# Performance work log

Hardware: AMD Instinct MI355X
Metric: run time of the kernel (lower is better)

## Reference

```python
import jax, jax.numpy as jnp
import numpy as np

D_MODEL = 1024
N_HEAD = 16


def setup_inputs() -> dict:
    key = jax.random.key(0)
    ks = jax.random.split(key, 12)
    B, T, D = 2, 2048, D_MODEL
    s = 1.0 / np.sqrt(D)
    return {
        "q": jax.random.normal(ks[0], (B, T, D), jnp.float32),
        "k": jax.random.normal(ks[1], (B, T, D), jnp.float32),
        "v": jax.random.normal(ks[2], (B, T, D), jnp.float32),
        "w_q": jax.random.normal(ks[3], (D, D), jnp.float32) * s,
        "b_q": jnp.zeros((D,), jnp.float32),
        "w_k": jax.random.normal(ks[4], (D, D), jnp.float32) * s,
        "b_k": jnp.zeros((D,), jnp.float32),
        "w_v": jax.random.normal(ks[5], (D, D), jnp.float32) * s,
        "b_v": jnp.zeros((D,), jnp.float32),
        "w_o": jax.random.normal(ks[6], (D, D), jnp.float32) * s,
        "b_o": jnp.zeros((D,), jnp.float32),
    }


def reference(q, k, v, w_q, b_q, w_k, b_k, w_v, b_v, w_o, b_o):
    B, T, D = q.shape
    H = N_HEAD
    nd = D // H  # head dim
    # projections (weights stored as [in, out])
    qh = (q @ w_q + b_q).reshape(B, T, H, nd).transpose(0, 2, 1, 3)  # [b,h,t,nd]
    kh = (k @ w_k + b_k).reshape(B, T, H, nd).transpose(0, 2, 1, 3)
    vh = (v @ w_v + b_v).reshape(B, T, H, nd).transpose(0, 2, 1, 3)
    score = jnp.einsum('bhqd,bhkd->bhqk', qh, kh) / jnp.sqrt(jnp.float32(nd))
    causal = jnp.tril(jnp.ones((T, T), dtype=bool))  # [tq, tk]
    score = jnp.where(causal, score, -jnp.inf)
    # NOTE: original module uses nn.Softmax(dim=-2), i.e. softmax over the
    # QUERY axis. Faithful to the source.
    attn = jax.nn.softmax(score, axis=-2)
    out = jnp.einsum('bhqk,bhkd->bhqd', attn, vh)  # [b,h,t,nd]
    out = out.transpose(0, 2, 1, 3).reshape(B, T, D)
    return out @ w_o + b_o
```

## Files before the change

### kernel.cpp

```cpp
#include <hip/hip_runtime.h>
#include <hip/hip_bf16.h>
#include <cstdint>
#include <cstddef>

#define D_MODEL 1024
#define NHEAD   16
#define HDIM    64
#define BB      2
#define TT      2048
#define MM      (BB*TT)
#define BHN     (BB*NHEAD)

typedef __attribute__((ext_vector_type(8))) __bf16 bf16x8;
typedef __attribute__((ext_vector_type(4))) float  f32x4;
typedef __attribute__((ext_vector_type(8))) unsigned short u16x8;
typedef __attribute__((ext_vector_type(4))) unsigned short u16x4;

__device__ __forceinline__ unsigned short f2b(float f){
  __bf16 b = (__bf16)f;
  return __builtin_bit_cast(unsigned short, b);
}
__device__ __forceinline__ float b2f(unsigned short u){
  unsigned int x = ((unsigned int)u) << 16;
  return __builtin_bit_cast(float, x);
}

__device__ __forceinline__ f32x4 mfma16(bf16x8 a, bf16x8 b, f32x4 c){
  return __builtin_amdgcn_mfma_f32_16x16x32_bf16(a, b, c, 0, 0, 0);
}

__device__ __forceinline__ void gload16(const void* g, void* lds){
  __builtin_amdgcn_global_load_lds((const __attribute__((address_space(1))) void*)g,
                                   (__attribute__((address_space(3))) void*)lds, 16, 0, 0);
}

__global__ void cvt_bf16_kernel(const float* __restrict__ q, const float* __restrict__ k,
                                const float* __restrict__ v,
                                unsigned short* __restrict__ Xq, unsigned short* __restrict__ Xk,
                                unsigned short* __restrict__ Xv){
  const int z = blockIdx.y;
  const float* x = z==0 ? q : z==1 ? k : v;
  unsigned short* y = z==0 ? Xq : z==1 ? Xk : Xv;
  size_t i = (size_t)blockIdx.x*blockDim.x + threadIdx.x;
  const float4* p = (const float4*)(x + i*8);
  float4 a = p[0], b = p[1];
  u16x8 o;
  o[0]=f2b(a.x); o[1]=f2b(a.y); o[2]=f2b(a.z); o[3]=f2b(a.w);
  o[4]=f2b(b.x); o[5]=f2b(b.y); o[6]=f2b(b.z); o[7]=f2b(b.w);
  *(u16x8*)(y + i*8) = o;
}

__global__ void transpose_w_kernel(const float* __restrict__ W0, const float* __restrict__ W1,
                                   const float* __restrict__ W2, const float* __restrict__ W3,
                                   unsigned short* __restrict__ T0, unsigned short* __restrict__ T1,
                                   unsigned short* __restrict__ T2, unsigned short* __restrict__ T3){
  __shared__ float tile[32][33];
  const int z = blockIdx.z;
  const float* W = z==0 ? W0 : z==1 ? W1 : z==2 ? W2 : W3;
  unsigned short* Wt = z==0 ? T0 : z==1 ? T1 : z==2 ? T2 : T3;
  int tx = threadIdx.x, ty = threadIdx.y;
  int x0 = blockIdx.x*32, y0 = blockIdx.y*32;
  #pragma unroll
  for (int i=0;i<4;i++)
    tile[ty + i*8][tx] = W[(size_t)(y0 + ty + i*8)*D_MODEL + x0 + tx];
  __syncthreads();
  #pragma unroll
  for (int i=0;i<4;i++)
    Wt[(size_t)(x0 + ty + i*8)*D_MODEL + y0 + tx] = f2b(tile[tx][ty + i*8]);
}

__device__ __forceinline__ void gemm_body(const unsigned short* __restrict__ A,
                                          const unsigned short* __restrict__ Bt,
                                          const float* __restrict__ bias,
                                          void* __restrict__ Cout, const int mode,
                                          const int m0, const int n0)
{
  constexpr int K = D_MODEL, N = D_MODEL;
  __shared__ unsigned short As[3][128*32];
  __shared__ unsigned short Bs[3][128*32];
  const int t = threadIdx.x, lane = t&63, w = t>>6;
  const int wr = w>>1, wc = w&1, lr = lane&15, lg = lane>>4;
  const int srow = lane>>2;
  const int schunk = (lane&3) ^ ((lane>>3)&3);
  const int crd = lg ^ ((lr>>1)&3);
  f32x4 acc[4][4] = {};

  auto stage = [&](int buf, int ks){
    int k0 = ks*32;
    #pragma unroll
    for (int g=0; g<2; g++){
      int reg = w*2 + g;
      int r = reg*16 + srow;
      gload16(A  + (size_t)(m0+r)*K + k0 + schunk*8, (char*)As[buf] + reg*1024);
      gload16(Bt + (size_t)(n0+r)*K + k0 + schunk*8, (char*)Bs[buf] + reg*1024);
    }
  };

  stage(0, 0);
  stage(1, 1);
  asm volatile("s_waitcnt vmcnt(4)" ::: "memory");
  asm volatile("s_barrier" ::: "memory");

  int bi = 0;
  for (int ks = 0; ks < 32; ++ks){
    if (ks + 2 < 32){
      int nb = bi + 2; if (nb >= 3) nb -= 3;
      stage(nb, ks+2);
    }
    const char* bufA = (const char*)As[bi];
    const char* bufB = (const char*)Bs[bi];
    bf16x8 af[4], bfv[4];
    #pragma unroll
    for (int mi=0;mi<4;mi++){
      int r = wr*64 + mi*16 + lr;
      af[mi] = *(const bf16x8*)(bufA + r*64 + crd*16);
    }
    #pragma unroll
    for (int ni=0;ni<4;ni++){
      int r = wc*64 + ni*16 + lr;
      bfv[ni] = *(const bf16x8*)(bufB + r*64 + crd*16);
    }
    #pragma unroll
    for (int mi=0;mi<4;mi++)
      #pragma unroll
      for (int ni=0;ni<4;ni++)
        acc[mi][ni] = mfma16(af[mi], bfv[ni], acc[mi][ni]);
    if (ks < 30) asm volatile("s_waitcnt vmcnt(4)" ::: "memory");
    else         asm volatile("s_waitcnt vmcnt(0)" ::: "memory");
    asm volatile("s_barrier" ::: "memory");
    bi = (bi == 2) ? 0 : bi + 1;
  }

  #pragma unroll
  for (int mi=0;mi<4;mi++){
    #pragma unroll
    for (int ni=0;ni<4;ni++){
      int n = n0 + wc*64 + ni*16 + lr;
      int mbase = m0 + wr*64 + mi*16 + lg*4;
      float bv = bias[n];
      if (mode == 0){
        unsigned short* Cb = (unsigned short*)Cout;
        #pragma unroll
        for (int r=0;r<4;r++) Cb[(size_t)(mbase+r)*N + n] = f2b(acc[mi][ni][r] + bv);
      } else {
        unsigned short* Vt = (unsigned short*)Cout;
        int h = n >> 6, d = n & 63;
        int b = mbase >> 11;
        int tq = mbase & (TT-1);
        u16x4 vv;
        #pragma unroll
        for (int r=0;r<4;r++) vv[r] = f2b(acc[mi][ni][r] + bv);
        *(u16x4*)(Vt + ((size_t)((b*NHEAD + h)*HDIM + d))*TT + tq) = vv;
      }
    }
  }
}

__launch_bounds__(256)
__global__ void proj_gemm_kernel(const unsigned short* __restrict__ Xq,
                                 const unsigned short* __restrict__ Xk,
                                 const unsigned short* __restrict__ Xv,
                                 const unsigned short* __restrict__ Wtq,
                                 const unsigned short* __restrict__ Wtk,
                                 const unsigned short* __restrict__ Wtv,
                                 const float* __restrict__ b_q, const float* __restrict__ b_k,
                                 const float* __restrict__ b_v,
                                 unsigned short* __restrict__ Qb, unsigned short* __restrict__ Kb,
                                 unsigned short* __restrict__ Vt)
{
  const int id = blockIdx.x;
  const int xcd = id & 7, r2 = id >> 3;
  const int n = r2 & 7, mz = r2 >> 3;
  const int m = (mz & 3)*8 + xcd, z = mz >> 2;
  const unsigned short* A  = z==0 ? Xq : z==1 ? Xk : Xv;
  const unsigned short* Bt = z==0 ? Wtq : z==1 ? Wtk : Wtv;
  const float* bias = z==0 ? b_q : z==1 ? b_k : b_v;
  void* C = z==0 ? (void*)Qb : z==1 ? (void*)Kb : (void*)Vt;
  gemm_body(A, Bt, bias, C, z==2 ? 1 : 0, m*128, n*128);
}

__launch_bounds__(256)
__global__ void out_gemm_kernel(const unsigned short* __restrict__ Ob,
                                const unsigned short* __restrict__ Wto,
                                const float* __restrict__ b_o, float* __restrict__ out)
{
  constexpr int K = D_MODEL, N = D_MODEL;
  __shared__ unsigned short As[2][64*32];
  __shared__ unsigned short Bs[2][128*32];
  const int id = blockIdx.x;
  const int xcd = id & 7, r2 = id >> 3;
  const int n0 = (r2 & 7)*128, m0 = ((r2 >> 3)*8 + xcd)*64;
  const int t = threadIdx.x, lane = t&63, w = t>>6;
  const int wr = w>>1, wc = w&1, lr = lane&15, lg = lane>>4;
  const int srow = lane>>2;
  const int schunk = (lane&3) ^ ((lane>>3)&3);
  const int crd = lg ^ ((lr>>1)&3);
  f32x4 acc[2][4] = {};

  auto stage = [&](int buf, int k0){
    { int r = w*16 + srow;
      gload16(Ob + (size_t)(m0+r)*K + k0 + schunk*8, (char*)As[buf] + w*1024); }
    #pragma unroll
    for (int g=0; g<2; g++){
      int reg = w*2 + g;
      int r = reg*16 + srow;
      gload16(Wto + (size_t)(n0+r)*K + k0 + schunk*8, (char*)Bs[buf] + reg*1024);
    }
  };

  stage(0, 0);
  __syncthreads();
  int buf = 0;
  for (int ks = 0; ks < 32; ++ks){
    if (ks < 31) stage(buf^1, (ks+1)*32);
    const char* bufA = (const char*)As[buf];
    const char* bufB = (const char*)Bs[buf];
    bf16x8 af[2], bfv[4];
    #pragma unroll
    for (int mi=0;mi<2;mi++){
      int r = wr*32 + mi*16 + lr;
      af[mi] = *(const bf16x8*)(bufA + r*64 + crd*16);
    }
    #pragma unroll
    for (int ni=0;ni<4;ni++){
      int r = wc*64 + ni*16 + lr;
      bfv[ni] = *(const bf16x8*)(bufB + r*64 + crd*16);
    }
    #pragma unroll
    for (int mi=0;mi<2;mi++)
      #pragma unroll
      for (int ni=0;ni<4;ni++)
        acc[mi][ni] = mfma16(af[mi], bfv[ni], acc[mi][ni]);
    __syncthreads();
    buf ^= 1;
  }

  #pragma unroll
  for (int mi=0;mi<2;mi++){
    #pragma unroll
    for (int ni=0;ni<4;ni++){
      int n = n0 + wc*64 + ni*16 + lr;
      int mbase = m0 + wr*32 + mi*16 + lg*4;
      float bv = b_o[n];
      #pragma unroll
      for (int r=0;r<4;r++) out[(size_t)(mbase+r)*N + n] = acc[mi][ni][r] + bv;
    }
  }
}

__launch_bounds__(256)
__global__ void col_stats_kernel(const unsigned short* __restrict__ Qb,
                                 const unsigned short* __restrict__ Kb,
                                 float* __restrict__ partialS)
{
  __shared__ unsigned short Ks[128*64];
  __shared__ unsigned short Qs[2][64*64];
  const int t = threadIdx.x, lane = t&63, w = t>>6;
  const int id = blockIdx.x;
  const int bh = id & 31, pair = id >> 5;
  const int kb_ = pair & 15, qc = pair >> 4;
  const int b = bh >> 4, h = bh & 15;
  const int k0 = kb_ * 128;
  const int lr = lane&15, lg = lane>>4;
  const int osrc = (lane&7) ^ (lane>>3);

  auto stageQ = [&](int buf, int qt){
    #pragma unroll
    for (int g=0; g<2; g++){
      int reg = w*2 + g;
      int r = reg*8 + (lane>>3);
      gload16(Qb + ((size_t)(b*TT + qt + r))*D_MODEL + h*64 + osrc*8,
              (char*)Qs[buf] + reg*1024);
    }
  };

  const int qstart = (k0 > qc*256) ? k0 : qc*256;
  const int qend   = (qc+1)*256;

  #pragma unroll
  for (int g=0; g<4; g++){
    int reg = w*4 + g;
    int r = reg*8 + (lane>>3);
    gload16(Kb + ((size_t)(b*TT + k0 + r))*D_MODEL + h*64 + osrc*8, (char*)Ks + reg*1024);
  }
  if (qstart < qend) stageQ(0, qstart);
  __syncthreads();

  bf16x8 bk[2][2];
  #pragma unroll
  for (int kb=0;kb<2;kb++)
    #pragma unroll
    for (int ks=0;ks<2;ks++){
      int r = w*32 + kb*16 + lr;
      bk[kb][ks] = *(const bf16x8*)((const char*)Ks + r*128 + (((ks*4+lg) ^ (r&7))*16));
    }
  f32x4 sacc[2] = {};
  int buf = 0;
  for (int qt = qstart; qt < qend; qt += 64){
    if (qt + 64 < qend) stageQ(buf^1, qt+64);
    const char* bufQ = (const char*)Qs[buf];
    const bool interior = (qt >= k0 + 128);
    #pragma unroll
    for (int qb=0;qb<4;qb++){
      bf16x8 aq[2];
      #pragma unroll
      for (int ks=0;ks<2;ks++){
        int r = qb*16 + lr;
        aq[ks] = *(const bf16x8*)(bufQ + r*128 + (((ks*4+lg) ^ (r&7))*16));
      }
      f32x4 sf[2] = {};
      #pragma unroll
      for (int ks=0;ks<2;ks++)
        #pragma unroll
        for (int kb=0;kb<2;kb++)
          sf[kb] = mfma16(aq[ks], bk[kb][ks], sf[kb]);
      #pragma unroll
      for (int kb=0;kb<2;kb++){
        int col = k0 + w*32 + kb*16 + lr;
        #pragma unroll
        for (int r=0;r<4;r++){
          float e = __expf(sf[kb][r] * 0.125f);
          if (!interior){
            int qg = qt + qb*16 + lg*4 + r;
            e = (qg >= col) ? e : 0.f;
          }
          sacc[kb][r] += e;
        }
      }
    }
    __syncthreads();
    buf ^= 1;
  }
  #pragma unroll
  for (int kb=0;kb<2;kb++){
    float s = sacc[kb][0] + sacc[kb][1] + sacc[kb][2] + sacc[kb][3];
    s += __shfl_xor(s, 16);
    s += __shfl_xor(s, 32);
    if (lg == 0){
      int col = k0 + w*32 + kb*16 + lr;
      partialS[((size_t)qc*BHN + bh)*TT + col] = s;
    }
  }
}

__global__ void col_combine_vscale_kernel(const float* __restrict__ partialS,
                                          unsigned short* __restrict__ Vt){
  const int bh = blockIdx.x >> 3, tc = blockIdx.x & 7;
  const int col = tc*256 + threadIdx.x;
  float s = 0.f;
  #pragma unroll
  for (int qc=0;qc<8;qc++) s += partialS[((size_t)qc*BHN + bh)*TT + col];
  const float inv = 1.0f / s;
  #pragma unroll 8
  for (int d=0; d<HDIM; d++){
    size_t idx = ((size_t)(bh*HDIM + d))*TT + col;
    Vt[idx] = f2b(b2f(Vt[idx]) * inv);
  }
}

__launch_bounds__(512)
__global__ void attn_out_kernel(const unsigned short* __restrict__ Qb,
                                const unsigned short* __restrict__ Kb,
                                const unsigned short* __restrict__ Vt,
                                unsigned short* __restrict__ O)
{
  __shared__ unsigned short Qs[128*64];
  __shared__ unsigned short Ks2[2][64*64];
  __shared__ unsigned short Vs[2][64*64];
  __shared__ unsigned short Ps[128*64];
  const int t = threadIdx.x, lane=t&63, w=t>>6;
  const int id = blockIdx.x;
  const int bh = id & 31;
  const int qi = 15 - (id >> 5);
  const int b = bh>>4, h = bh&15;
  const int q0 = qi*128;
  const int lr = lane&15, lg = lane>>4;
  const int osrc = (lane&7) ^ (lane>>3);

  auto stageKV = [&](int buf, int k0){
    int r = w*8 + (lane>>3);
    gload16(Kb + ((size_t)(b*TT + k0 + r))*D_MODEL + h*64 + osrc*8,
            (char*)Ks2[buf] + w*1024);
    gload16(Vt + ((size_t)(bh*HDIM + r))*TT + k0 + osrc*8,
            (char*)Vs[buf] + w*1024);
  };

  #pragma unroll
  for (int g=0; g<2; g++){
    int reg = w*2 + g;
    int r = reg*8 + (lane>>3);
    gload16(Qb + ((size_t)(b*TT + q0 + r))*D_MODEL + h*64 + osrc*8, (char*)Qs + reg*1024);
  }
  stageKV(0, 0);
  __syncthreads();

  bf16x8 aq[2];
  #pragma unroll
  for (int ks=0;ks<2;ks++){
    int r = w*16 + lr;
    aq[ks] = *(const bf16x8*)((const char*)Qs + r*128 + (((ks*4+lg) ^ (r&7))*16));
  }
  f32x4 oacc[4] = {};
  const int nkt = 2*qi + 2;
  int buf = 0;
  for (int kt=0; kt<nkt; kt++){
    int k0 = kt*64;
    if (kt+1 < nkt) stageKV(buf^1, k0+64);
    const bool active = (k0 <= q0 + w*16 + 15);
    if (active){
      const char* bufK = (const char*)Ks2[buf];
      const char* bufV = (const char*)Vs[buf];
      f32x4 sf[4] = {};
      __builtin_amdgcn_s_setprio(1);
      #pragma unroll
      for (int ks=0;ks<2;ks++)
        #pragma unroll
        for (int kb=0;kb<4;kb++){
          int r = kb*16 + lr;
          bf16x8 bk = *(const bf16x8*)(bufK + r*128 + (((ks*4+lg) ^ (r&7))*16));
          sf[kb] = mfma16(bk, aq[ks], sf[kb]);
        }
      __builtin_amdgcn_s_setprio(0);
      const bool boundary = (k0 + 64 > q0 + w*16);
      const int prow = w*16 + lr;
      #pragma unroll
      for (int kb=0;kb<4;kb++){
        u16x4 vv;
        #pragma unroll
        for (int r=0;r<4;r++){
          float pv = __expf(sf[kb][r]*0.125f);
          if (boundary){
            int kg = k0 + kb*16 + lg*4 + r;
            int qg = q0 + prow;
            pv = (qg >= kg) ? pv : 0.f;
          }
          vv[r] = f2b(pv);
        }
        *(u16x4*)((char*)Ps + ((prow*128 + kb*32 + lg*8) ^ ((prow&7)<<4))) = vv;
      }
      __builtin_amdgcn_s_setprio(1);
      #pragma unroll
      for (int ks=0;ks<2;ks++){
        bf16x8 pa = *(const bf16x8*)((const char*)Ps + prow*128 + (((ks*4+lg) ^ (prow&7))*16));
        #pragma unroll
        for (int db=0;db<4;db++){
          int r = db*16 + lr;
          bf16x8 bv = *(const bf16x8*)(bufV + r*128 + (((ks*4+lg) ^ (r&7))*16));
          oacc[db] = mfma16(pa, bv, oacc[db]);
        }
      }
      __builtin_amdgcn_s_setprio(0);
    }
    __syncthreads();
    buf ^= 1;
  }
  #pragma unroll
  for (int db=0;db<4;db++){
    int qg = q0 + w*16 + lg*4;
    int d  = db*16 + lr;
    #pragma unroll
    for (int r=0;r<4;r++)
      O[((size_t)(b*TT + qg + r))*D_MODEL + h*64 + d] = f2b(oacc[db][r]);
  }
}

extern "C" void kernel_launch(void* const* d_in, const int* in_sizes, int n_in,
                              void* d_out, int out_size, void* d_ws, size_t ws_size,
                              hipStream_t stream)
{
  (void)in_sizes; (void)n_in; (void)out_size; (void)ws_size;
  const float* q   = (const float*)d_in[0];
  const float* k   = (const float*)d_in[1];
  const float* v   = (const float*)d_in[2];
  const float* w_q = (const float*)d_in[3];
  const float* b_q = (const float*)d_in[4];
  const float* w_k = (const float*)d_in[5];
  const float* b_k = (const float*)d_in[6];
  const float* w_v = (const float*)d_in[7];
  const float* b_v = (const float*)d_in[8];
  const float* w_o = (const float*)d_in[9];
  const float* b_o = (const float*)d_in[10];

  char* p = (char*)d_ws;
  auto carve = [&](size_t bytes)->char* {
    char* r = p; p += (bytes + 255) & ~(size_t)255; return r;
  };
  unsigned short* Xq  = (unsigned short*)carve((size_t)MM*D_MODEL*2);
  unsigned short* Xk  = (unsigned short*)carve((size_t)MM*D_MODEL*2);
  unsigned short* Xv  = (unsigned short*)carve((size_t)MM*D_MODEL*2);
  unsigned short* Wtq = (unsigned short*)carve((size_t)D_MODEL*D_MODEL*2);
  unsigned short* Wtk = (unsigned short*)carve((size_t)D_MODEL*D_MODEL*2);
  unsigned short* Wtv = (unsigned short*)carve((size_t)D_MODEL*D_MODEL*2);
  unsigned short* Wto = (unsigned short*)carve((size_t)D_MODEL*D_MODEL*2);
  unsigned short* Qb  = (unsigned short*)carve((size_t)MM*D_MODEL*2);
  unsigned short* Kb  = (unsigned short*)carve((size_t)MM*D_MODEL*2);
  unsigned short* Vt  = (unsigned short*)carve((size_t)MM*D_MODEL*2);
  unsigned short* Ob  = (unsigned short*)carve((size_t)MM*D_MODEL*2);
  float* partialS = (float*)carve((size_t)8*BHN*TT*4);

  cvt_bf16_kernel<<<dim3((MM*D_MODEL/8)/256, 3), 256, 0, stream>>>(q, k, v, Xq, Xk, Xv);

  dim3 tgrid(32,32,4), tblk(32,8);
  transpose_w_kernel<<<tgrid, tblk, 0, stream>>>(w_q, w_k, w_v, w_o, Wtq, Wtk, Wtv, Wto);

  proj_gemm_kernel<<<dim3(768), 256, 0, stream>>>(Xq, Xk, Xv, Wtq, Wtk, Wtv,
                                                  b_q, b_k, b_v, Qb, Kb, Vt);

  col_stats_kernel<<<dim3(8*16*BHN), 256, 0, stream>>>(Qb, Kb, partialS);
  col_combine_vscale_kernel<<<dim3(BHN*8), 256, 0, stream>>>(partialS, Vt);

  attn_out_kernel<<<dim3((TT/128)*BHN), 512, 0, stream>>>(Qb, Kb, Vt, Ob);

  out_gemm_kernel<<<dim3(512), 256, 0, stream>>>(Ob, Wto, b_o, (float*)d_out);
}
```

Baseline: 147.3 us.

## Fuse preprocessing kernels, fold column normalization into attention, simplify GEMM pipeline

Merges the bf16 conversion and weight transpose into one launch. Removes the separate column-combine/V-scaling kernel: the attention kernel now sums the per-chunk column partials into a shared-memory reciprocal table and multiplies each P entry by it, instead of rescaling V in memory. The GEMM body drops from a triple-buffered pipeline with manual vmcnt waits to double-buffering with __syncthreads, which lowers LDS use but exposes more load latency. The reciprocal table adds 8KB of LDS to the attention kernel and every block recomputes its own column sums, duplicating that work.

```diff
diff --git a/kernel.cpp b/kernel.cpp
--- a/kernel.cpp
+++ b/kernel.cpp
@@ -20,10 +20,6 @@
   __bf16 b = (__bf16)f;
   return __builtin_bit_cast(unsigned short, b);
 }
-__device__ __forceinline__ float b2f(unsigned short u){
-  unsigned int x = ((unsigned int)u) << 16;
-  return __builtin_bit_cast(float, x);
-}
 
 __device__ __forceinline__ f32x4 mfma16(bf16x8 a, bf16x8 b, f32x4 c){
   return __builtin_amdgcn_mfma_f32_16x16x32_bf16(a, b, c, 0, 0, 0);
@@ -34,39 +30,44 @@
                                    (__attribute__((address_space(3))) void*)lds, 16, 0, 0);
 }
 
-__global__ void cvt_bf16_kernel(const float* __restrict__ q, const float* __restrict__ k,
-                                const float* __restrict__ v,
-                                unsigned short* __restrict__ Xq, unsigned short* __restrict__ Xk,
-                                unsigned short* __restrict__ Xv){
-  const int z = blockIdx.y;
-  const float* x = z==0 ? q : z==1 ? k : v;
-  unsigned short* y = z==0 ? Xq : z==1 ? Xk : Xv;
-  size_t i = (size_t)blockIdx.x*blockDim.x + threadIdx.x;
-  const float4* p = (const float4*)(x + i*8);
-  float4 a = p[0], b = p[1];
-  u16x8 o;
-  o[0]=f2b(a.x); o[1]=f2b(a.y); o[2]=f2b(a.z); o[3]=f2b(a.w);
-  o[4]=f2b(b.x); o[5]=f2b(b.y); o[6]=f2b(b.z); o[7]=f2b(b.w);
-  *(u16x8*)(y + i*8) = o;
-}
-
-__global__ void transpose_w_kernel(const float* __restrict__ W0, const float* __restrict__ W1,
-                                   const float* __restrict__ W2, const float* __restrict__ W3,
-                                   unsigned short* __restrict__ T0, unsigned short* __restrict__ T1,
-                                   unsigned short* __restrict__ T2, unsigned short* __restrict__ T3){
+__global__ void pre_kernel(const float* __restrict__ q, const float* __restrict__ k,
+                           const float* __restrict__ v,
+                           unsigned short* __restrict__ Xq, unsigned short* __restrict__ Xk,
+                           unsigned short* __restrict__ Xv,
+                           const float* __restrict__ W0, const float* __restrict__ W1,
+                           const float* __restrict__ W2, const float* __restrict__ W3,
+                           unsigned short* __restrict__ T0, unsigned short* __restrict__ T1,
+                           unsigned short* __restrict__ T2, unsigned short* __restrict__ T3)
+{
   __shared__ float tile[32][33];
-  const int z = blockIdx.z;
-  const float* W = z==0 ? W0 : z==1 ? W1 : z==2 ? W2 : W3;
-  unsigned short* Wt = z==0 ? T0 : z==1 ? T1 : z==2 ? T2 : T3;
-  int tx = threadIdx.x, ty = threadIdx.y;
-  int x0 = blockIdx.x*32, y0 = blockIdx.y*32;
-  #pragma unroll
-  for (int i=0;i<4;i++)
-    tile[ty + i*8][tx] = W[(size_t)(y0 + ty + i*8)*D_MODEL + x0 + tx];
-  __syncthreads();
-  #pragma unroll
-  for (int i=0;i<4;i++)
-    Wt[(size_t)(x0 + ty + i*8)*D_MODEL + y0 + tx] = f2b(tile[tx][ty + i*8]);
+  const int id = blockIdx.x;
+  if (id < 6144){
+    const int z = id / 2048, ib = id - z*2048;
+    const float* x = z==0 ? q : z==1 ? k : v;
+    unsigned short* y = z==0 ? Xq : z==1 ? Xk : Xv;
+    size_t i = (size_t)ib*256 + threadIdx.x;
+    const float4* p = (const float4*)(x + i*8);
+    float4 a = p[0], b = p[1];
+    u16x8 o;
+    o[0]=f2b(a.x); o[1]=f2b(a.y); o[2]=f2b(a.z); o[3]=f2b(a.w);
+    o[4]=f2b(b.x); o[5]=f2b(b.y); o[6]=f2b(b.z); o[7]=f2b(b.w);
+    *(u16x8*)(y + i*8) = o;
+  } else {
+    const int tid = id - 6144;
+    const int z = tid >> 10;
+    const int by = (tid >> 5) & 31, bx = tid & 31;
+    const float* W = z==0 ? W0 : z==1 ? W1 : z==2 ? W2 : W3;
+    unsigned short* Wt = z==0 ? T0 : z==1 ? T1 : z==2 ? T2 : T3;
+    const int tx = threadIdx.x & 31, ty = threadIdx.x >> 5;
+    const int x0 = bx*32, y0 = by*32;
+    #pragma unroll
+    for (int i=0;i<4;i++)
+      tile[ty + i*8][tx] = W[(size_t)(y0 + ty + i*8)*D_MODEL + x0 + tx];
+    __syncthreads();
+    #pragma unroll
+    for (int i=0;i<4;i++)
+      Wt[(size_t)(x0 + ty + i*8)*D_MODEL + y0 + tx] = f2b(tile[tx][ty + i*8]);
+  }
 }
 
 __device__ __forceinline__ void gemm_body(const unsigned short* __restrict__ A,
@@ -76,8 +77,8 @@
                                           const int m0, const int n0)
 {
   constexpr int K = D_MODEL, N = D_MODEL;
-  __shared__ unsigned short As[3][128*32];
-  __shared__ unsigned short Bs[3][128*32];
+  __shared__ unsigned short As[2][128*32];
+  __shared__ unsigned short Bs[2][128*32];
   const int t = threadIdx.x, lane = t&63, w = t>>6;
   const int wr = w>>1, wc = w&1, lr = lane&15, lg = lane>>4;
   const int srow = lane>>2;
@@ -85,8 +86,7 @@
   const int crd = lg ^ ((lr>>1)&3);
   f32x4 acc[4][4] = {};
 
-  auto stage = [&](int buf, int ks){
-    int k0 = ks*32;
+  auto stage = [&](int buf, int k0){
     #pragma unroll
     for (int g=0; g<2; g++){
       int reg = w*2 + g;
@@ -97,18 +97,12 @@
   };
 
   stage(0, 0);
-  stage(1, 1);
-  asm volatile("s_waitcnt vmcnt(4)" ::: "memory");
-  asm volatile("s_barrier" ::: "memory");
-
-  int bi = 0;
+  __syncthreads();
+  int buf = 0;
   for (int ks = 0; ks < 32; ++ks){
-    if (ks + 2 < 32){
-      int nb = bi + 2; if (nb >= 3) nb -= 3;
-      stage(nb, ks+2);
-    }
-    const char* bufA = (const char*)As[bi];
-    const char* bufB = (const char*)Bs[bi];
+    if (ks < 31) stage(buf^1, (ks+1)*32);
+    const char* bufA = (const char*)As[buf];
+    const char* bufB = (const char*)Bs[buf];
     bf16x8 af[4], bfv[4];
     #pragma unroll
     for (int mi=0;mi<4;mi++){
@@ -125,10 +119,8 @@
       #pragma unroll
       for (int ni=0;ni<4;ni++)
         acc[mi][ni] = mfma16(af[mi], bfv[ni], acc[mi][ni]);
-    if (ks < 30) asm volatile("s_waitcnt vmcnt(4)" ::: "memory");
-    else         asm volatile("s_waitcnt vmcnt(0)" ::: "memory");
-    asm volatile("s_barrier" ::: "memory");
-    bi = (bi == 2) ? 0 : bi + 1;
+    __syncthreads();
+    buf ^= 1;
   }
 
   #pragma unroll
@@ -343,31 +335,18 @@
   }
 }
 
-__global__ void col_combine_vscale_kernel(const float* __restrict__ partialS,
-                                          unsigned short* __restrict__ Vt){
-  const int bh = blockIdx.x >> 3, tc = blockIdx.x & 7;
-  const int col = tc*256 + threadIdx.x;
-  float s = 0.f;
-  #pragma unroll
-  for (int qc=0;qc<8;qc++) s += partialS[((size_t)qc*BHN + bh)*TT + col];
-  const float inv = 1.0f / s;
-  #pragma unroll 8
-  for (int d=0; d<HDIM; d++){
-    size_t idx = ((size_t)(bh*HDIM + d))*TT + col;
-    Vt[idx] = f2b(b2f(Vt[idx]) * inv);
-  }
-}
-
 __launch_bounds__(512)
 __global__ void attn_out_kernel(const unsigned short* __restrict__ Qb,
                                 const unsigned short* __restrict__ Kb,
                                 const unsigned short* __restrict__ Vt,
+                                const float* __restrict__ partialS,
                                 unsigned short* __restrict__ O)
 {
   __shared__ unsigned short Qs[128*64];
   __shared__ unsigned short Ks2[2][64*64];
   __shared__ unsigned short Vs[2][64*64];
   __shared__ unsigned short Ps[128*64];
+  __shared__ float inv_s[TT];
   const int t = threadIdx.x, lane=t&63, w=t>>6;
   const int id = blockIdx.x;
   const int bh = id & 31;
@@ -392,6 +371,14 @@
     gload16(Qb + ((size_t)(b*TT + q0 + r))*D_MODEL + h*64 + osrc*8, (char*)Qs + reg*1024);
   }
   stageKV(0, 0);
+
+  const int ncols = q0 + 128;
+  for (int c = t; c < ncols; c += 512){
+    float s = 0.f;
+    #pragma unroll
+    for (int qc=0;qc<8;qc++) s += partialS[((size_t)qc*BHN + bh)*TT + c];
+    inv_s[c] = 1.0f / s;
+  }
   __syncthreads();
 
   bf16x8 aq[2];
@@ -425,10 +412,11 @@
       const int prow = w*16 + lr;
       #pragma unroll
       for (int kb=0;kb<4;kb++){
+        f32x4 inv4 = *(const f32x4*)&inv_s[k0 + kb*16 + lg*4];
         u16x4 vv;
         #pragma unroll
         for (int r=0;r<4;r++){
-          float pv = __expf(sf[kb][r]*0.125f);
+          float pv = __expf(sf[kb][r]*0.125f) * inv4[r];
           if (boundary){
             int kg = k0 + kb*16 + lg*4 + r;
             int qg = q0 + prow;
@@ -498,18 +486,16 @@
   unsigned short* Ob  = (unsigned short*)carve((size_t)MM*D_MODEL*2);
   float* partialS = (float*)carve((size_t)8*BHN*TT*4);
 
-  cvt_bf16_kernel<<<dim3((MM*D_MODEL/8)/256, 3), 256, 0, stream>>>(q, k, v, Xq, Xk, Xv);
-
-  dim3 tgrid(32,32,4), tblk(32,8);
-  transpose_w_kernel<<<tgrid, tblk, 0, stream>>>(w_q, w_k, w_v, w_o, Wtq, Wtk, Wtv, Wto);
+  pre_kernel<<<dim3(6144 + 4096), 256, 0, stream>>>(q, k, v, Xq, Xk, Xv,
+                                                    w_q, w_k, w_v, w_o,
+                                                    Wtq, Wtk, Wtv, Wto);
 
   proj_gemm_kernel<<<dim3(768), 256, 0, stream>>>(Xq, Xk, Xv, Wtq, Wtk, Wtv,
                                                   b_q, b_k, b_v, Qb, Kb, Vt);
 
   col_stats_kernel<<<dim3(8*16*BHN), 256, 0, stream>>>(Qb, Kb, partialS);
-  col_combine_vscale_kernel<<<dim3(BHN*8), 256, 0, stream>>>(partialS, Vt);
-
-  attn_out_kernel<<<dim3((TT/128)*BHN), 512, 0, stream>>>(Qb, Kb, Vt, Ob);
+
+  attn_out_kernel<<<dim3((TT/128)*BHN), 512, 0, stream>>>(Qb, Kb, Vt, partialS, Ob);
 
   out_gemm_kernel<<<dim3(512), 256, 0, stream>>>(Ob, Wto, b_o, (float*)d_out);
 }
```

Result: faster. 142.6 us (-3.2%).
